# Kernel tuning notes

Hardware: AMD Instinct MI355X
Metric: run time of the kernel (lower is better)

## Reference

```python
import jax, jax.numpy as jnp
import numpy as np

H = 8   # num_heads
K = 4   # sampling points per head


def setup_inputs() -> dict:
    key = jax.random.key(0)
    ks = jax.random.split(key, 12)
    B, T, Lv, C = 4, 8, 9216, 256
    Lq = 9216
    s = 0.02
    inp = {
        "Fp": jax.random.normal(ks[0], (B, T, Lv, C), jnp.float32),
        "queries": jax.random.normal(ks[1], (B, Lq, C), jnp.float32),
        "idx_q": jax.random.randint(ks[2], (B, Lq), 0, Lv, jnp.int32),
        "t_ref_q": jax.random.uniform(ks[3], (B, Lq), jnp.float32) * (T - 1),
        # learned params (torch nn.Linear: y = x @ W.T + b; store as [in, out])
        "W_off": jax.random.normal(ks[4], (C, H * K), jnp.float32) * s,
        "b_off": jnp.zeros((H * K,), jnp.float32),
        "W_attn": jax.random.normal(ks[5], (C, H * K), jnp.float32) * s,
        "b_attn": jax.random.normal(ks[6], (H * K,), jnp.float32) * s,
        "W_v": jax.random.normal(ks[7], (C, C), jnp.float32) * s,
        "b_v": jax.random.normal(ks[8], (C,), jnp.float32) * s,
        "W_out": jax.random.normal(ks[9], (C, C), jnp.float32) * s,
        "b_out": jax.random.normal(ks[10], (C,), jnp.float32) * s,
    }
    return inp


def reference(Fp, queries, idx_q, t_ref_q,
              W_off, b_off, W_attn, b_attn, W_v, b_v, W_out, b_out):
    B, T, Lv, C = Fp.shape
    _, Lq, _ = queries.shape
    hd = C // H  # head_dim

    # value projection, split into heads: [B,T,Lv,H,hd]
    V = (jnp.einsum('btlc,cd->btld', Fp, W_v) + b_v).reshape(B, T, Lv, H, hd)

    offsets = (queries @ W_off + b_off).reshape(B, Lq, H, K)
    attn_logits = (queries @ W_attn + b_attn).reshape(B, Lq, H, K)
    attn_weights = jax.nn.softmax(attn_logits, axis=-1)          # [B,Lq,H,K]

    t_sample = jnp.clip(t_ref_q[:, :, None, None] + offsets, 0.0, float(T - 1))
    t0 = jnp.floor(t_sample).astype(jnp.int32)                    # [B,Lq,H,K]
    t1 = jnp.minimum(t0 + 1, T - 1)
    alpha = (t_sample - t0.astype(t_sample.dtype))[..., None]     # [B,Lq,H,K,1]

    b_idx = jnp.arange(B)[:, None, None, None]                    # [B,1,1,1]
    h_idx = jnp.arange(H)[None, None, :, None]                    # [1,1,H,1]
    idx_exp = idx_q.astype(jnp.int32)[:, :, None, None]           # [B,Lq,1,1]

    # per-head temporal gather: [B,Lq,H,K,hd]
    v0 = V[b_idx, t0, idx_exp, h_idx]
    v1 = V[b_idx, t1, idx_exp, h_idx]
    sampled = (1.0 - alpha) * v0 + alpha * v1

    head_out = jnp.einsum('blhk,blhkd->blhd', attn_weights, sampled)
    head_out = head_out.reshape(B, Lq, C)
    return head_out @ W_out + b_out
```

## Files before the change

kernel.cpp:

```cpp
#include <hip/hip_runtime.h>
#include <hip/hip_bf16.h>

#define HH 8
#define KK 4
#define CC 256
#define TT 8
#define LQV 9216

typedef __attribute__((ext_vector_type(8))) short bf16x8;
typedef __attribute__((ext_vector_type(4))) float f32x4;

#define MFMA16(a, b, c) __builtin_amdgcn_mfma_f32_16x16x32_bf16(a, b, c, 0, 0, 0)

__device__ __forceinline__ unsigned short f2bf(float f) {
    union { float f; unsigned u; } v; v.f = f;
    unsigned r = v.u + 0x7fffu + ((v.u >> 16) & 1u);
    return (unsigned short)(r >> 16);
}
__device__ __forceinline__ float bf2f(unsigned short s) {
    union { unsigned u; float f; } v; v.u = ((unsigned)s) << 16;
    return v.f;
}

__global__ void k0_prep(const float* __restrict__ Wv, const float* __restrict__ Wout,
                        const float* __restrict__ Woff, const float* __restrict__ Wattn,
                        int* __restrict__ flags, int* __restrict__ count,
                        unsigned short* __restrict__ WvT, unsigned short* __restrict__ WoutT,
                        unsigned short* __restrict__ WoaT,
                        int nrows, int blocks_flags)
{
    const int tid = threadIdx.x;
    if ((int)blockIdx.x < blocks_flags) {
        const int gid = blockIdx.x * 256 + tid;
        if (gid < nrows) flags[gid] = 0;
        if (gid == 0) count[0] = 0;
        return;
    }
    int o = (blockIdx.x - blocks_flags) * 256 + tid;
    if (o < 65536) { int d = o >> 8, c = o & 255; WvT[o]   = f2bf(Wv[c * 256 + d]);   return; }
    o -= 65536;
    if (o < 65536) { int d = o >> 8, c = o & 255; WoutT[o] = f2bf(Wout[c * 256 + d]); return; }
    o -= 65536;
    if (o < 16384) {
        int n = o >> 8, c = o & 255;
        WoaT[o] = f2bf(n < 32 ? Woff[c * 32 + n] : Wattn[c * 32 + (n - 32)]);
    }
}

__launch_bounds__(256, 2)
__global__ void k1b_offlog(const float* __restrict__ queries, const unsigned short* __restrict__ WoaT,
                           const float* __restrict__ b_off, const float* __restrict__ b_attn,
                           float* __restrict__ offlog)
{
    __shared__ __attribute__((aligned(16))) unsigned short A_s[128 * 48];
    __shared__ __attribute__((aligned(16))) unsigned short B_s[64 * 48];
    const int tid = threadIdx.x;
    const int q0 = blockIdx.x * 128;
    const int wid = tid >> 6, l = tid & 63;
    const int wm = wid >> 1, wn = wid & 1;

    f32x4 acc[4][2];
    #pragma unroll
    for (int i = 0; i < 4; ++i)
        #pragma unroll
        for (int j = 0; j < 2; ++j) acc[i][j] = (f32x4){0.f, 0.f, 0.f, 0.f};

    const int arow = tid >> 1, ahalf = tid & 1;
    const int brow = tid >> 2, bq = tid & 3;
    const float* asrc = queries + (size_t)(q0 + arow) * CC + ahalf * 16;

    for (int ks = 0; ks < 8; ++ks) {
        const int k0 = ks * 32;
        {
            float4 v0 = *(const float4*)(asrc + k0);
            float4 v1 = *(const float4*)(asrc + k0 + 4);
            float4 v2 = *(const float4*)(asrc + k0 + 8);
            float4 v3 = *(const float4*)(asrc + k0 + 12);
            bf16x8 p0, p1;
            p0[0]=f2bf(v0.x); p0[1]=f2bf(v0.y); p0[2]=f2bf(v0.z); p0[3]=f2bf(v0.w);
            p0[4]=f2bf(v1.x); p0[5]=f2bf(v1.y); p0[6]=f2bf(v1.z); p0[7]=f2bf(v1.w);
            p1[0]=f2bf(v2.x); p1[1]=f2bf(v2.y); p1[2]=f2bf(v2.z); p1[3]=f2bf(v2.w);
            p1[4]=f2bf(v3.x); p1[5]=f2bf(v3.y); p1[6]=f2bf(v3.z); p1[7]=f2bf(v3.w);
            *(bf16x8*)&A_s[arow * 48 + ahalf * 16]     = p0;
            *(bf16x8*)&A_s[arow * 48 + ahalf * 16 + 8] = p1;
        }
        {
            if (brow < 64)
                *(bf16x8*)&B_s[brow * 48 + bq * 8] =
                    *(const bf16x8*)&WoaT[brow * 256 + k0 + bq * 8];
        }
        __syncthreads();
        bf16x8 af[4], bfv[2];
        const int kb = (l >> 4) * 8, r0 = wm * 64 + (l & 15), c0 = wn * 32 + (l & 15);
        #pragma unroll
        for (int am = 0; am < 4; ++am) af[am] = *(bf16x8*)&A_s[(r0 + am * 16) * 48 + kb];
        #pragma unroll
        for (int bn = 0; bn < 2; ++bn) bfv[bn] = *(bf16x8*)&B_s[(c0 + bn * 16) * 48 + kb];
        #pragma unroll
        for (int am = 0; am < 4; ++am)
            #pragma unroll
            for (int bn = 0; bn < 2; ++bn)
                acc[am][bn] = MFMA16(af[am], bfv[bn], acc[am][bn]);
        __syncthreads();
    }
    #pragma unroll
    for (int bn = 0; bn < 2; ++bn) {
        const int col = wn * 32 + bn * 16 + (l & 15);
        const float bias = (col < 32) ? b_off[col] : b_attn[col - 32];
        #pragma unroll
        for (int am = 0; am < 4; ++am)
            #pragma unroll
            for (int j = 0; j < 4; ++j) {
                const int row = q0 + wm * 64 + am * 16 + (l >> 4) * 4 + j;
                offlog[(size_t)row * 64 + col] = acc[am][bn][j] + bias;
            }
    }
}

__global__ void k0c_coef(const float* __restrict__ offlog, const int* __restrict__ idx_q,
                         const float* __restrict__ t_ref_q,
                         float* __restrict__ coefW, int* __restrict__ amaskW,
                         int* __restrict__ flags, int nq)
{
    const int q = blockIdx.x * 256 + threadIdx.x;
    if (q >= nq) return;
    const int b = q / LQV;
    const int idx = idx_q[q];
    const float tr = t_ref_q[q];
    const float* ol = offlog + (size_t)q * 64;
    int am = 0;
    #pragma unroll
    for (int h = 0; h < HH; ++h) {
        float4 offv = *(const float4*)(ol + h * 4);
        float4 lgv  = *(const float4*)(ol + 32 + h * 4);
        float off[KK] = {offv.x, offv.y, offv.z, offv.w};
        float lg[KK]  = {lgv.x, lgv.y, lgv.z, lgv.w};
        float m = fmaxf(fmaxf(lg[0], lg[1]), fmaxf(lg[2], lg[3]));
        float e[KK], s = 0.f;
        #pragma unroll
        for (int k = 0; k < KK; ++k) { e[k] = expf(lg[k] - m); s += e[k]; }
        const float inv = 1.f / s;
        float crow[TT] = {0.f,0.f,0.f,0.f,0.f,0.f,0.f,0.f};
        #pragma unroll
        for (int k = 0; k < KK; ++k) {
            const float w = e[k] * inv;
            float ts = fminf(fmaxf(tr + off[k], 0.f), (float)(TT - 1));
            const int t0 = (int)ts;
            const int t1 = min(t0 + 1, TT - 1);
            const float a = ts - (float)t0;
            const float w0 = w * (1.f - a), w1 = w * a;
            #pragma unroll
            for (int t = 0; t < TT; ++t)
                crow[t] += ((t == t0) ? w0 : 0.f) + ((t == t1) ? w1 : 0.f);
            am |= (1 << t0) | (1 << t1);
        }
        float4 c0 = {crow[0], crow[1], crow[2], crow[3]};
        float4 c1 = {crow[4], crow[5], crow[6], crow[7]};
        *(float4*)&coefW[(size_t)q * 64 + h * 8]     = c0;
        *(float4*)&coefW[(size_t)q * 64 + h * 8 + 4] = c1;
    }
    amaskW[q] = am;
    const int base = b * (TT * LQV) + idx;
    #pragma unroll
    for (int t = 0; t < TT; ++t)
        if ((am >> t) & 1) flags[base + t * LQV] = 1;
}

__global__ void k0d_compact(const int* __restrict__ flags, int* __restrict__ count,
                            int* __restrict__ list, int nrows)
{
    const int i = blockIdx.x * 256 + threadIdx.x;
    const bool p = (i < nrows) && (flags[i] != 0);
    const unsigned long long m = __ballot(p);
    const int lane = threadIdx.x & 63;
    const int lc = __popcll(m & ((1ull << lane) - 1ull));
    int base = 0;
    if (lane == 0) base = atomicAdd(count, __popcll(m));
    base = __shfl(base, 0);
    if (p) list[base + lc] = i;
}

__launch_bounds__(512, 2)
__global__ void k1_zgemm(const float* __restrict__ Fp, const unsigned short* __restrict__ WvT,
                         const int* __restrict__ count, const int* __restrict__ list,
                         unsigned short* __restrict__ Z)
{
    __shared__ __attribute__((aligned(16))) unsigned short A_s[128 * 48];
    __shared__ __attribute__((aligned(16))) unsigned short B_s[256 * 48];
    __shared__ int rows_s[128];
    const int cnt = count[0];
    const int bm0 = blockIdx.x * 128;
    if (bm0 >= cnt) return;
    const int tid = threadIdx.x;
    if (tid < 128) {
        const int i = bm0 + tid;
        rows_s[tid] = (i < cnt) ? list[i] : -1;
    }
    __syncthreads();
    const int wid = tid >> 6, l = tid & 63;
    const int wm = wid >> 2, wn = wid & 3;

    f32x4 acc[4][4];
    #pragma unroll
    for (int i = 0; i < 4; ++i)
        #pragma unroll
        for (int j = 0; j < 4; ++j) acc[i][j] = (f32x4){0.f, 0.f, 0.f, 0.f};

    const int arow = tid >> 2, aq = tid & 3;
    const int brow = tid >> 1, bh = tid & 1;
    int rho = rows_s[arow]; if (rho < 0) rho = 0;
    const float* asrc = Fp + (size_t)rho * CC + aq * 8;

    for (int ks = 0; ks < 8; ++ks) {
        const int k0 = ks * 32;
        {
            float4 v0 = *(const float4*)(asrc + k0);
            float4 v1 = *(const float4*)(asrc + k0 + 4);
            bf16x8 p;
            p[0]=f2bf(v0.x); p[1]=f2bf(v0.y); p[2]=f2bf(v0.z); p[3]=f2bf(v0.w);
            p[4]=f2bf(v1.x); p[5]=f2bf(v1.y); p[6]=f2bf(v1.z); p[7]=f2bf(v1.w);
            *(bf16x8*)&A_s[arow * 48 + aq * 8] = p;
        }
        {
            *(bf16x8*)&B_s[brow * 48 + bh * 16]     = *(const bf16x8*)&WvT[brow * 256 + k0 + bh * 16];
            *(bf16x8*)&B_s[brow * 48 + bh * 16 + 8] = *(const bf16x8*)&WvT[brow * 256 + k0 + bh * 16 + 8];
        }
        __syncthreads();
        bf16x8 af[4], bfv[4];
        const int kb = (l >> 4) * 8, r0 = wm * 64 + (l & 15), c0 = wn * 64 + (l & 15);
        #pragma unroll
        for (int am = 0; am < 4; ++am) af[am] = *(bf16x8*)&A_s[(r0 + am * 16) * 48 + kb];
        #pragma unroll
        for (int bn = 0; bn < 4; ++bn) bfv[bn] = *(bf16x8*)&B_s[(c0 + bn * 16) * 48 + kb];
        #pragma unroll
        for (int am = 0; am < 4; ++am)
            #pragma unroll
            for (int bn = 0; bn < 4; ++bn)
                acc[am][bn] = MFMA16(af[am], bfv[bn], acc[am][bn]);
        __syncthreads();
    }
    #pragma unroll
    for (int am = 0; am < 4; ++am) {
        #pragma unroll
        for (int j = 0; j < 4; ++j) {
            const int trow = wm * 64 + am * 16 + (l >> 4) * 4 + j;
            const int r = rows_s[trow];
            if (r < 0) continue;
            #pragma unroll
            for (int bn = 0; bn < 4; ++bn) {
                const int col = wn * 64 + bn * 16 + (l & 15);
                Z[(size_t)r * CC + col] = f2bf(acc[am][bn][j]);
            }
        }
    }
}

__launch_bounds__(256, 4)
__global__ void k2_final(const unsigned short* __restrict__ Z, const float* __restrict__ coefW,
                         const int* __restrict__ amaskW, const int* __restrict__ idx_q,
                         const unsigned short* __restrict__ WoutT,
                         const float* __restrict__ b_v, const float* __restrict__ b_out,
                         float* __restrict__ out)
{
    __shared__ float coef_s[16 * 64];
    __shared__ __attribute__((aligned(16))) unsigned short ho_s[16 * 264];
    __shared__ int am_s[16];
    __shared__ int base_s[16];
    const int tid = threadIdx.x;
    const int q0 = blockIdx.x * 16;

    for (int i = tid; i < 1024; i += 256) coef_s[i] = coefW[(size_t)q0 * 64 + i];
    if (tid < 16) {
        const int q = q0 + tid;
        am_s[tid] = amaskW[q];
        const int b = q / LQV;
        base_s[tid] = b * (TT * LQV) + idx_q[q];
    }
    __syncthreads();

    const float bv = b_v[tid];
    const int h8 = (tid >> 5) * 8;
    float ho[16];
    #pragma unroll
    for (int iq = 0; iq < 16; ++iq) {
        float acc = bv;
        const int am = am_s[iq];
        const int base = base_s[iq];
        const float* cf = &coef_s[iq * 64 + h8];
        #pragma unroll
        for (int t = 0; t < TT; ++t) {
            if ((am >> t) & 1) {
                const float z = bf2f(Z[(size_t)(base + t * LQV) * CC + tid]);
                acc += cf[t] * z;
            }
        }
        ho[iq] = acc;
    }
    #pragma unroll
    for (int iq = 0; iq < 16; ++iq) ho_s[iq * 264 + tid] = f2bf(ho[iq]);
    __syncthreads();

    const int wid = tid >> 6, l = tid & 63;
    const int kb = (l >> 4) * 8, r = l & 15;
    f32x4 acc[4];
    #pragma unroll
    for (int nt = 0; nt < 4; ++nt) acc[nt] = (f32x4){0.f, 0.f, 0.f, 0.f};
    for (int ks = 0; ks < 8; ++ks) {
        const bf16x8 a = *(bf16x8*)&ho_s[r * 264 + ks * 32 + kb];
        #pragma unroll
        for (int nt = 0; nt < 4; ++nt) {
            const int col = (wid * 4 + nt) * 16 + r;
            const bf16x8 bfr = *(const bf16x8*)&WoutT[(size_t)col * 256 + ks * 32 + kb];
            acc[nt] = MFMA16(a, bfr, acc[nt]);
        }
    }
    #pragma unroll
    for (int nt = 0; nt < 4; ++nt) {
        const int col = (wid * 4 + nt) * 16 + r;
        const float bo = b_out[col];
        #pragma unroll
        for (int j = 0; j < 4; ++j) {
            const int row = (l >> 4) * 4 + j;
            out[(size_t)(q0 + row) * CC + col] = acc[nt][j] + bo;
        }
    }
}

#define QB 8
__launch_bounds__(256, 2)
__global__ void tda_fused(const float* __restrict__ Fp, const float* __restrict__ queries,
                          const int* __restrict__ idx_q, const float* __restrict__ t_ref_q,
                          const float* __restrict__ W_off, const float* __restrict__ b_off,
                          const float* __restrict__ W_attn, const float* __restrict__ b_attn,
                          const float* __restrict__ W_v, const float* __restrict__ b_v,
                          const float* __restrict__ W_out, const float* __restrict__ b_out,
                          float* __restrict__ out, int Lv)
{
    __shared__ __attribute__((aligned(16))) float g_s[QB][HH][CC];
    __shared__ __attribute__((aligned(16))) float qho_s[QB][CC];
    __shared__ float offlog[QB][64];
    __shared__ float coef[QB][HH][TT];
    __shared__ float tref_s[QB];
    __shared__ int idx_s[QB];
    __shared__ int amask[QB];
    const int tid = threadIdx.x;
    const long qbase = (long)blockIdx.x * QB;
    const int b = (int)(qbase / LQV);
    #pragma unroll
    for (int i = 0; i < QB; ++i) qho_s[i][tid] = queries[(qbase + i) * CC + tid];
    if (tid < QB) { tref_s[tid] = t_ref_q[qbase + tid]; idx_s[tid] = idx_q[qbase + tid]; amask[tid] = 0; }
    { float* cf = &coef[0][0][0]; cf[tid] = 0.f; cf[tid + 256] = 0.f; }
    __syncthreads();
    {
        const int o = tid & 63, i0 = tid >> 6, col = o & 31;
        const float* W = (o < 32) ? W_off : W_attn;
        const float bias = (o < 32) ? b_off[col] : b_attn[col];
        float acc0 = 0.f, acc1 = 0.f;
        for (int c = 0; c < CC; ++c) {
            const float w = W[c * 32 + col];
            acc0 += qho_s[i0][c] * w; acc1 += qho_s[i0 + 4][c] * w;
        }
        offlog[i0][o] = acc0 + bias; offlog[i0 + 4][o] = acc1 + bias;
    }
    __syncthreads();
    if (tid < QB * HH) {
        const int i = tid >> 3, h = tid & 7;
        float off[KK], lg[KK];
        #pragma unroll
        for (int k = 0; k < KK; ++k) { off[k] = offlog[i][h * KK + k]; lg[k] = offlog[i][32 + h * KK + k]; }
        float m = fmaxf(fmaxf(lg[0], lg[1]), fmaxf(lg[2], lg[3]));
        float e[KK], s = 0.f;
        #pragma unroll
        for (int k = 0; k < KK; ++k) { e[k] = expf(lg[k] - m); s += e[k]; }
        const float inv = 1.f / s;
        const float tr = tref_s[i];
        int mask = 0;
        #pragma unroll
        for (int k = 0; k < KK; ++k) {
            const float w = e[k] * inv;
            float ts = fminf(fmaxf(tr + off[k], 0.f), (float)(TT - 1));
            const int t0 = (int)ts; const int t1 = min(t0 + 1, TT - 1);
            const float a = ts - (float)t0;
            coef[i][h][t0] += w * (1.f - a); coef[i][h][t1] += w * a;
            mask |= (1 << t0) | (1 << t1);
        }
        atomicOr(&amask[i], mask);
    }
    __syncthreads();
    for (int i = 0; i < QB; ++i) {
        float g[HH] = {0.f,0.f,0.f,0.f,0.f,0.f,0.f,0.f};
        const int am = amask[i]; const int idx = idx_s[i];
        for (int t = 0; t < TT; ++t) {
            if ((am >> t) & 1) {
                const float rv = Fp[((long)(b * TT + t) * Lv + idx) * CC + tid];
                #pragma unroll
                for (int h = 0; h < HH; ++h) g[h] += coef[i][h][t] * rv;
            }
        }
        #pragma unroll
        for (int h = 0; h < HH; ++h) g_s[i][h][tid] = g[h];
    }
    __syncthreads();
    {
        const int h = tid >> 5;
        float acc[QB];
        #pragma unroll
        for (int i = 0; i < QB; ++i) acc[i] = b_v[tid];
        for (int c = 0; c < CC; c += 4) {
            const float w0 = W_v[(c + 0) * CC + tid], w1 = W_v[(c + 1) * CC + tid];
            const float w2 = W_v[(c + 2) * CC + tid], w3 = W_v[(c + 3) * CC + tid];
            #pragma unroll
            for (int i = 0; i < QB; ++i) {
                const float4 gv = *reinterpret_cast<const float4*>(&g_s[i][h][c]);
                acc[i] += gv.x * w0 + gv.y * w1 + gv.z * w2 + gv.w * w3;
            }
        }
        __syncthreads();
        #pragma unroll
        for (int i = 0; i < QB; ++i) qho_s[i][tid] = acc[i];
    }
    __syncthreads();
    {
        float acc[QB];
        #pragma unroll
        for (int i = 0; i < QB; ++i) acc[i] = b_out[tid];
        for (int c = 0; c < CC; c += 4) {
            const float w0 = W_out[(c + 0) * CC + tid], w1 = W_out[(c + 1) * CC + tid];
            const float w2 = W_out[(c + 2) * CC + tid], w3 = W_out[(c + 3) * CC + tid];
            #pragma unroll
            for (int i = 0; i < QB; ++i) {
                const float4 hv = *reinterpret_cast<const float4*>(&qho_s[i][c]);
                acc[i] += hv.x * w0 + hv.y * w1 + hv.z * w2 + hv.w * w3;
            }
        }
        #pragma unroll
        for (int i = 0; i < QB; ++i) out[(qbase + i) * CC + tid] = acc[i];
    }
}

extern "C" void kernel_launch(void* const* d_in, const int* in_sizes, int n_in,
                              void* d_out, int out_size, void* d_ws, size_t ws_size,
                              hipStream_t stream) {
    const float* Fp      = (const float*)d_in[0];
    const float* queries = (const float*)d_in[1];
    const int*   idx_q   = (const int*)d_in[2];
    const float* t_ref   = (const float*)d_in[3];
    const float* W_off   = (const float*)d_in[4];
    const float* b_off   = (const float*)d_in[5];
    const float* W_attn  = (const float*)d_in[6];
    const float* b_attn  = (const float*)d_in[7];
    const float* W_v     = (const float*)d_in[8];
    const float* b_v     = (const float*)d_in[9];
    const float* W_out   = (const float*)d_in[10];
    const float* b_out   = (const float*)d_in[11];
    float* out = (float*)d_out;

    const int nq    = in_sizes[2];
    const int Bdim  = nq / LQV;
    const int nrows = Bdim * TT * LQV;

    size_t cur = 0;
    auto alloc = [&](size_t bytes) { size_t o = cur; cur += (bytes + 255) & ~(size_t)255; return o; };
    const size_t o_Z      = alloc((size_t)nrows * CC * 2);
    const size_t o_offlog = alloc((size_t)nq * 64 * 4);
    const size_t o_coef   = alloc((size_t)nq * 64 * 4);
    const size_t o_amask  = alloc((size_t)nq * 4);
    const size_t o_flags  = alloc((size_t)nrows * 4);
    const size_t o_list   = alloc((size_t)nrows * 4);
    const size_t o_count  = alloc(256);
    const size_t o_WvT    = alloc(65536 * 2);
    const size_t o_WoutT  = alloc(65536 * 2);
    const size_t o_WoaT   = alloc(16384 * 2);
    const size_t need = cur;

    if (ws_size < need) {
        tda_fused<<<nq / QB, 256, 0, stream>>>(Fp, queries, idx_q, t_ref,
                                               W_off, b_off, W_attn, b_attn,
                                               W_v, b_v, W_out, b_out, out, LQV);
        return;
    }

    char* ws = (char*)d_ws;
    unsigned short* Z     = (unsigned short*)(ws + o_Z);
    float* offlog         = (float*)(ws + o_offlog);
    float* coefW          = (float*)(ws + o_coef);
    int*   amaskW         = (int*)(ws + o_amask);
    int*   flags          = (int*)(ws + o_flags);
    int*   list           = (int*)(ws + o_list);
    int*   count          = (int*)(ws + o_count);
    unsigned short* WvT   = (unsigned short*)(ws + o_WvT);
    unsigned short* WoutT = (unsigned short*)(ws + o_WoutT);
    unsigned short* WoaT  = (unsigned short*)(ws + o_WoaT);

    const int blocks_flags = (nrows + 255) / 256;
    const int grid_prep = blocks_flags + 256 + 256 + 64;
    k0_prep<<<grid_prep, 256, 0, stream>>>(W_v, W_out, W_off, W_attn,
                                           flags, count, WvT, WoutT, WoaT,
                                           nrows, blocks_flags);
    k1b_offlog<<<nq / 128, 256, 0, stream>>>(queries, WoaT, b_off, b_attn, offlog);
    k0c_coef<<<(nq + 255) / 256, 256, 0, stream>>>(offlog, idx_q, t_ref,
                                                   coefW, amaskW, flags, nq);
    k0d_compact<<<blocks_flags, 256, 0, stream>>>(flags, count, list, nrows);
    k1_zgemm<<<(nrows + 127) / 128, 512, 0, stream>>>(Fp, WvT, count, list, Z);
    k2_final<<<nq / 16, 256, 0, stream>>>(Z, coefW, amaskW, idx_q, WoutT,
                                          b_v, b_out, out);
}
```

Measured before the change: 205.1 us.

## Fuse offset/logit GEMM with coefficient computation and vectorize Z gather

The offset/attention-logit GEMM now writes its results to shared memory, and the same block computes the softmax, temporal interpolation coefficients and row flags, so the global offlog buffer and one kernel launch are gone. Flag and count zeroing moves to hipMemsetAsync. LDS row padding changes from 48 to 40 elements in the GEMM kernels. The final kernel's Z gather is vectorized to 8 bf16 values per thread with uint4 loads and float4 coefficient staging. The fused block leaves only half its threads active during the coefficient phase, and the padding change may alter LDS bank conflicts.

Result: faster. 184.7 us (-10.0%).

```diff
diff --git a/kernel.cpp b/kernel.cpp
--- a/kernel.cpp
+++ b/kernel.cpp
@@ -24,19 +24,10 @@
 
 __global__ void k0_prep(const float* __restrict__ Wv, const float* __restrict__ Wout,
                         const float* __restrict__ Woff, const float* __restrict__ Wattn,
-                        int* __restrict__ flags, int* __restrict__ count,
                         unsigned short* __restrict__ WvT, unsigned short* __restrict__ WoutT,
-                        unsigned short* __restrict__ WoaT,
-                        int nrows, int blocks_flags)
+                        unsigned short* __restrict__ WoaT)
 {
-    const int tid = threadIdx.x;
-    if ((int)blockIdx.x < blocks_flags) {
-        const int gid = blockIdx.x * 256 + tid;
-        if (gid < nrows) flags[gid] = 0;
-        if (gid == 0) count[0] = 0;
-        return;
-    }
-    int o = (blockIdx.x - blocks_flags) * 256 + tid;
+    int o = blockIdx.x * 256 + threadIdx.x;
     if (o < 65536) { int d = o >> 8, c = o & 255; WvT[o]   = f2bf(Wv[c * 256 + d]);   return; }
     o -= 65536;
     if (o < 65536) { int d = o >> 8, c = o & 255; WoutT[o] = f2bf(Wout[c * 256 + d]); return; }
@@ -48,12 +39,17 @@
 }
 
 __launch_bounds__(256, 2)
-__global__ void k1b_offlog(const float* __restrict__ queries, const unsigned short* __restrict__ WoaT,
-                           const float* __restrict__ b_off, const float* __restrict__ b_attn,
-                           float* __restrict__ offlog)
+__global__ void k1b_offcoef(const float* __restrict__ queries, const unsigned short* __restrict__ WoaT,
+                            const float* __restrict__ b_off, const float* __restrict__ b_attn,
+                            const int* __restrict__ idx_q, const float* __restrict__ t_ref_q,
+                            float* __restrict__ coefW, int* __restrict__ amaskW,
+                            int* __restrict__ flags)
 {
-    __shared__ __attribute__((aligned(16))) unsigned short A_s[128 * 48];
-    __shared__ __attribute__((aligned(16))) unsigned short B_s[64 * 48];
+    __shared__ __attribute__((aligned(16))) char smem[128 * 65 * 4];
+    unsigned short* A_s = (unsigned short*)smem;
+    unsigned short* B_s = (unsigned short*)(smem + 128 * 40 * 2);
+    float* olog = (float*)smem;
+
     const int tid = threadIdx.x;
     const int q0 = blockIdx.x * 128;
     const int wid = tid >> 6, l = tid & 63;
@@ -81,21 +77,20 @@
             p0[4]=f2bf(v1.x); p0[5]=f2bf(v1.y); p0[6]=f2bf(v1.z); p0[7]=f2bf(v1.w);
             p1[0]=f2bf(v2.x); p1[1]=f2bf(v2.y); p1[2]=f2bf(v2.z); p1[3]=f2bf(v2.w);
             p1[4]=f2bf(v3.x); p1[5]=f2bf(v3.y); p1[6]=f2bf(v3.z); p1[7]=f2bf(v3.w);
-            *(bf16x8*)&A_s[arow * 48 + ahalf * 16]     = p0;
-            *(bf16x8*)&A_s[arow * 48 + ahalf * 16 + 8] = p1;
+            *(bf16x8*)&A_s[arow * 40 + ahalf * 16]     = p0;
+            *(bf16x8*)&A_s[arow * 40 + ahalf * 16 + 8] = p1;
         }
         {
-            if (brow < 64)
-                *(bf16x8*)&B_s[brow * 48 + bq * 8] =
-                    *(const bf16x8*)&WoaT[brow * 256 + k0 + bq * 8];
+            *(bf16x8*)&B_s[brow * 40 + bq * 8] =
+                *(const bf16x8*)&WoaT[brow * 256 + k0 + bq * 8];
         }
         __syncthreads();
         bf16x8 af[4], bfv[2];
         const int kb = (l >> 4) * 8, r0 = wm * 64 + (l & 15), c0 = wn * 32 + (l & 15);
         #pragma unroll
-        for (int am = 0; am < 4; ++am) af[am] = *(bf16x8*)&A_s[(r0 + am * 16) * 48 + kb];
-        #pragma unroll
-        for (int bn = 0; bn < 2; ++bn) bfv[bn] = *(bf16x8*)&B_s[(c0 + bn * 16) * 48 + kb];
+        for (int am = 0; am < 4; ++am) af[am] = *(bf16x8*)&A_s[(r0 + am * 16) * 40 + kb];
+        #pragma unroll
+        for (int bn = 0; bn < 2; ++bn) bfv[bn] = *(bf16x8*)&B_s[(c0 + bn * 16) * 40 + kb];
         #pragma unroll
         for (int am = 0; am < 4; ++am)
             #pragma unroll
@@ -103,6 +98,7 @@
                 acc[am][bn] = MFMA16(af[am], bfv[bn], acc[am][bn]);
         __syncthreads();
     }
+
     #pragma unroll
     for (int bn = 0; bn < 2; ++bn) {
         const int col = wn * 32 + bn * 16 + (l & 15);
@@ -111,59 +107,54 @@
         for (int am = 0; am < 4; ++am)
             #pragma unroll
             for (int j = 0; j < 4; ++j) {
-                const int row = q0 + wm * 64 + am * 16 + (l >> 4) * 4 + j;
-                offlog[(size_t)row * 64 + col] = acc[am][bn][j] + bias;
-            }
-    }
-}
-
-__global__ void k0c_coef(const float* __restrict__ offlog, const int* __restrict__ idx_q,
-                         const float* __restrict__ t_ref_q,
-                         float* __restrict__ coefW, int* __restrict__ amaskW,
-                         int* __restrict__ flags, int nq)
-{
-    const int q = blockIdx.x * 256 + threadIdx.x;
-    if (q >= nq) return;
-    const int b = q / LQV;
-    const int idx = idx_q[q];
-    const float tr = t_ref_q[q];
-    const float* ol = offlog + (size_t)q * 64;
-    int am = 0;
-    #pragma unroll
-    for (int h = 0; h < HH; ++h) {
-        float4 offv = *(const float4*)(ol + h * 4);
-        float4 lgv  = *(const float4*)(ol + 32 + h * 4);
-        float off[KK] = {offv.x, offv.y, offv.z, offv.w};
-        float lg[KK]  = {lgv.x, lgv.y, lgv.z, lgv.w};
-        float m = fmaxf(fmaxf(lg[0], lg[1]), fmaxf(lg[2], lg[3]));
-        float e[KK], s = 0.f;
-        #pragma unroll
-        for (int k = 0; k < KK; ++k) { e[k] = expf(lg[k] - m); s += e[k]; }
-        const float inv = 1.f / s;
-        float crow[TT] = {0.f,0.f,0.f,0.f,0.f,0.f,0.f,0.f};
-        #pragma unroll
-        for (int k = 0; k < KK; ++k) {
-            const float w = e[k] * inv;
-            float ts = fminf(fmaxf(tr + off[k], 0.f), (float)(TT - 1));
-            const int t0 = (int)ts;
-            const int t1 = min(t0 + 1, TT - 1);
-            const float a = ts - (float)t0;
-            const float w0 = w * (1.f - a), w1 = w * a;
-            #pragma unroll
-            for (int t = 0; t < TT; ++t)
-                crow[t] += ((t == t0) ? w0 : 0.f) + ((t == t1) ? w1 : 0.f);
-            am |= (1 << t0) | (1 << t1);
-        }
-        float4 c0 = {crow[0], crow[1], crow[2], crow[3]};
-        float4 c1 = {crow[4], crow[5], crow[6], crow[7]};
-        *(float4*)&coefW[(size_t)q * 64 + h * 8]     = c0;
-        *(float4*)&coefW[(size_t)q * 64 + h * 8 + 4] = c1;
-    }
-    amaskW[q] = am;
-    const int base = b * (TT * LQV) + idx;
-    #pragma unroll
-    for (int t = 0; t < TT; ++t)
-        if ((am >> t) & 1) flags[base + t * LQV] = 1;
+                const int lr = wm * 64 + am * 16 + (l >> 4) * 4 + j;
+                olog[lr * 65 + col] = acc[am][bn][j] + bias;
+            }
+    }
+    __syncthreads();
+
+    if (tid < 128) {
+        const int q = q0 + tid;
+        const int b = q / LQV;
+        const int idx = idx_q[q];
+        const float tr = t_ref_q[q];
+        const float* ol = olog + tid * 65;
+        int am = 0;
+        #pragma unroll
+        for (int h = 0; h < HH; ++h) {
+            float off[KK], lg[KK];
+            #pragma unroll
+            for (int k = 0; k < KK; ++k) { off[k] = ol[h * 4 + k]; lg[k] = ol[32 + h * 4 + k]; }
+            float m = fmaxf(fmaxf(lg[0], lg[1]), fmaxf(lg[2], lg[3]));
+            float e[KK], s = 0.f;
+            #pragma unroll
+            for (int k = 0; k < KK; ++k) { e[k] = expf(lg[k] - m); s += e[k]; }
+            const float inv = 1.f / s;
+            float crow[TT] = {0.f,0.f,0.f,0.f,0.f,0.f,0.f,0.f};
+            #pragma unroll
+            for (int k = 0; k < KK; ++k) {
+                const float w = e[k] * inv;
+                float ts = fminf(fmaxf(tr + off[k], 0.f), (float)(TT - 1));
+                const int t0 = (int)ts;
+                const int t1 = min(t0 + 1, TT - 1);
+                const float a = ts - (float)t0;
+                const float w0 = w * (1.f - a), w1 = w * a;
+                #pragma unroll
+                for (int t = 0; t < TT; ++t)
+                    crow[t] += ((t == t0) ? w0 : 0.f) + ((t == t1) ? w1 : 0.f);
+                am |= (1 << t0) | (1 << t1);
+            }
+            float4 c0 = {crow[0], crow[1], crow[2], crow[3]};
+            float4 c1 = {crow[4], crow[5], crow[6], crow[7]};
+            *(float4*)&coefW[(size_t)q * 64 + h * 8]     = c0;
+            *(float4*)&coefW[(size_t)q * 64 + h * 8 + 4] = c1;
+        }
+        amaskW[q] = am;
+        const int base = b * (TT * LQV) + idx;
+        #pragma unroll
+        for (int t = 0; t < TT; ++t)
+            if ((am >> t) & 1) flags[base + t * LQV] = 1;
+    }
 }
 
 __global__ void k0d_compact(const int* __restrict__ flags, int* __restrict__ count,
@@ -185,8 +176,8 @@
                          const int* __restrict__ count, const int* __restrict__ list,
                          unsigned short* __restrict__ Z)
 {
-    __shared__ __attribute__((aligned(16))) unsigned short A_s[128 * 48];
-    __shared__ __attribute__((aligned(16))) unsigned short B_s[256 * 48];
+    __shared__ __attribute__((aligned(16))) unsigned short A_s[128 * 40];
+    __shared__ __attribute__((aligned(16))) unsigned short B_s[256 * 40];
     __shared__ int rows_s[128];
     const int cnt = count[0];
     const int bm0 = blockIdx.x * 128;
@@ -219,19 +210,19 @@
             bf16x8 p;
             p[0]=f2bf(v0.x); p[1]=f2bf(v0.y); p[2]=f2bf(v0.z); p[3]=f2bf(v0.w);
             p[4]=f2bf(v1.x); p[5]=f2bf(v1.y); p[6]=f2bf(v1.z); p[7]=f2bf(v1.w);
-            *(bf16x8*)&A_s[arow * 48 + aq * 8] = p;
+            *(bf16x8*)&A_s[arow * 40 + aq * 8] = p;
         }
         {
-            *(bf16x8*)&B_s[brow * 48 + bh * 16]     = *(const bf16x8*)&WvT[brow * 256 + k0 + bh * 16];
-            *(bf16x8*)&B_s[brow * 48 + bh * 16 + 8] = *(const bf16x8*)&WvT[brow * 256 + k0 + bh * 16 + 8];
+            *(bf16x8*)&B_s[brow * 40 + bh * 16]     = *(const bf16x8*)&WvT[brow * 256 + k0 + bh * 16];
+            *(bf16x8*)&B_s[brow * 40 + bh * 16 + 8] = *(const bf16x8*)&WvT[brow * 256 + k0 + bh * 16 + 8];
         }
         __syncthreads();
         bf16x8 af[4], bfv[4];
         const int kb = (l >> 4) * 8, r0 = wm * 64 + (l & 15), c0 = wn * 64 + (l & 15);
         #pragma unroll
-        for (int am = 0; am < 4; ++am) af[am] = *(bf16x8*)&A_s[(r0 + am * 16) * 48 + kb];
-        #pragma unroll
-        for (int bn = 0; bn < 4; ++bn) bfv[bn] = *(bf16x8*)&B_s[(c0 + bn * 16) * 48 + kb];
+        for (int am = 0; am < 4; ++am) af[am] = *(bf16x8*)&A_s[(r0 + am * 16) * 40 + kb];
+        #pragma unroll
+        for (int bn = 0; bn < 4; ++bn) bfv[bn] = *(bf16x8*)&B_s[(c0 + bn * 16) * 40 + kb];
         #pragma unroll
         for (int am = 0; am < 4; ++am)
             #pragma unroll
@@ -262,42 +253,58 @@
                          const float* __restrict__ b_v, const float* __restrict__ b_out,
                          float* __restrict__ out)
 {
-    __shared__ float coef_s[16 * 64];
+    __shared__ float coef_s[16 * 68];
     __shared__ __attribute__((aligned(16))) unsigned short ho_s[16 * 264];
     __shared__ int am_s[16];
     __shared__ int base_s[16];
     const int tid = threadIdx.x;
     const int q0 = blockIdx.x * 16;
 
-    for (int i = tid; i < 1024; i += 256) coef_s[i] = coefW[(size_t)q0 * 64 + i];
-    if (tid < 16) {
-        const int q = q0 + tid;
-        am_s[tid] = amaskW[q];
-        const int b = q / LQV;
-        base_s[tid] = b * (TT * LQV) + idx_q[q];
-    }
-    __syncthreads();
-
-    const float bv = b_v[tid];
-    const int h8 = (tid >> 5) * 8;
-    float ho[16];
-    #pragma unroll
-    for (int iq = 0; iq < 16; ++iq) {
-        float acc = bv;
+    if (tid < 128) {
+        const int iq = tid >> 3, qd = tid & 7;
+        const float4 v0 = *(const float4*)&coefW[(size_t)(q0 + iq) * 64 + qd * 8];
+        const float4 v1 = *(const float4*)&coefW[(size_t)(q0 + iq) * 64 + qd * 8 + 4];
+        *(float4*)&coef_s[iq * 68 + qd * 8]     = v0;
+        *(float4*)&coef_s[iq * 68 + qd * 8 + 4] = v1;
+    } else if (tid < 144) {
+        const int i = tid - 128;
+        const int q = q0 + i;
+        am_s[i] = amaskW[q];
+        base_s[i] = (q / LQV) * (TT * LQV) + idx_q[q];
+    }
+    __syncthreads();
+
+    const int g = tid & 31;
+    const int iq0 = tid >> 5;
+    const float4 bv0 = *(const float4*)&b_v[g * 8];
+    const float4 bv1 = *(const float4*)&b_v[g * 8 + 4];
+    #pragma unroll
+    for (int p = 0; p < 2; ++p) {
+        const int iq = iq0 + 8 * p;
         const int am = am_s[iq];
         const int base = base_s[iq];
-        const float* cf = &coef_s[iq * 64 + h8];
+        const float* cf = &coef_s[iq * 68 + (g >> 2) * 8];
+        float acc[8] = {bv0.x, bv0.y, bv0.z, bv0.w, bv1.x, bv1.y, bv1.z, bv1.w};
         #pragma unroll
         for (int t = 0; t < TT; ++t) {
             if ((am >> t) & 1) {
-                const float z = bf2f(Z[(size_t)(base + t * LQV) * CC + tid]);
-                acc += cf[t] * z;
-            }
-        }
-        ho[iq] = acc;
-    }
-    #pragma unroll
-    for (int iq = 0; iq < 16; ++iq) ho_s[iq * 264 + tid] = f2bf(ho[iq]);
+                const float c = cf[t];
+                const uint4 zv = *(const uint4*)&Z[(size_t)(base + t * LQV) * CC + g * 8];
+                acc[0] += c * bf2f((unsigned short)(zv.x & 0xffffu));
+                acc[1] += c * bf2f((unsigned short)(zv.x >> 16));
+                acc[2] += c * bf2f((unsigned short)(zv.y & 0xffffu));
+                acc[3] += c * bf2f((unsigned short)(zv.y >> 16));
+                acc[4] += c * bf2f((unsigned short)(zv.z & 0xffffu));
+                acc[5] += c * bf2f((unsigned short)(zv.z >> 16));
+                acc[6] += c * bf2f((unsigned short)(zv.w & 0xffffu));
+                acc[7] += c * bf2f((unsigned short)(zv.w >> 16));
+            }
+        }
+        bf16x8 hp;
+        #pragma unroll
+        for (int j = 0; j < 8; ++j) hp[j] = (short)f2bf(acc[j]);
+        *(bf16x8*)&ho_s[iq * 264 + g * 8] = hp;
+    }
     __syncthreads();
 
     const int wid = tid >> 6, l = tid & 63;
@@ -462,7 +469,6 @@
     size_t cur = 0;
     auto alloc = [&](size_t bytes) { size_t o = cur; cur += (bytes + 255) & ~(size_t)255; return o; };
     const size_t o_Z      = alloc((size_t)nrows * CC * 2);
-    const size_t o_offlog = alloc((size_t)nq * 64 * 4);
     const size_t o_coef   = alloc((size_t)nq * 64 * 4);
     const size_t o_amask  = alloc((size_t)nq * 4);
     const size_t o_flags  = alloc((size_t)nrows * 4);
@@ -482,7 +488,6 @@
 
     char* ws = (char*)d_ws;
     unsigned short* Z     = (unsigned short*)(ws + o_Z);
-    float* offlog         = (float*)(ws + o_offlog);
     float* coefW          = (float*)(ws + o_coef);
     int*   amaskW         = (int*)(ws + o_amask);
     int*   flags          = (int*)(ws + o_flags);
@@ -492,15 +497,13 @@
     unsigned short* WoutT = (unsigned short*)(ws + o_WoutT);
     unsigned short* WoaT  = (unsigned short*)(ws + o_WoaT);
 
-    const int blocks_flags = (nrows + 255) / 256;
-    const int grid_prep = blocks_flags + 256 + 256 + 64;
-    k0_prep<<<grid_prep, 256, 0, stream>>>(W_v, W_out, W_off, W_attn,
-                                           flags, count, WvT, WoutT, WoaT,
-                                           nrows, blocks_flags);
-    k1b_offlog<<<nq / 128, 256, 0, stream>>>(queries, WoaT, b_off, b_attn, offlog);
-    k0c_coef<<<(nq + 255) / 256, 256, 0, stream>>>(offlog, idx_q, t_ref,
-                                                   coefW, amaskW, flags, nq);
-    k0d_compact<<<blocks_flags, 256, 0, stream>>>(flags, count, list, nrows);
+    hipMemsetAsync(flags, 0, (size_t)nrows * 4, stream);
+    hipMemsetAsync(count, 0, 4, stream);
+
+    k0_prep<<<576, 256, 0, stream>>>(W_v, W_out, W_off, W_attn, WvT, WoutT, WoaT);
+    k1b_offcoef<<<nq / 128, 256, 0, stream>>>(queries, WoaT, b_off, b_attn,
+                                              idx_q, t_ref, coefW, amaskW, flags);
+    k0d_compact<<<(nrows + 255) / 256, 256, 0, stream>>>(flags, count, list, nrows);
     k1_zgemm<<<(nrows + 127) / 128, 512, 0, stream>>>(Fp, WvT, count, list, Z);
     k2_final<<<nq / 16, 256, 0, stream>>>(Z, coefW, amaskW, idx_q, WoutT,
                                           b_v, b_out, out);
```
